# Performance work log

Hardware: AMD Instinct MI355X
Metric: run time of the kernel (lower is better)

The kernel has to match this reference:

```python
import jax, jax.numpy as jnp
import numpy as np

VOCAB = 50257
D_MODEL = 256
HIDDEN = 512
NUM_CLASSES = 2
BATCH = 64
SEQ = 512
PAD_IDX = 0


def setup_inputs() -> dict:
    key = jax.random.key(0)
    ks = jax.random.split(key, 8)
    input_ids = jax.random.randint(ks[0], (BATCH, SEQ), 0, VOCAB)
    emb = jax.random.normal(ks[1], (VOCAB, D_MODEL), dtype=jnp.float32) * 0.02
    emb = emb.at[PAD_IDX].set(0.0)  # padding_idx row is zero
    s_x = 1.0 / np.sqrt(D_MODEL)
    s_h = 1.0 / np.sqrt(HIDDEN)
    Wx = jax.random.uniform(ks[2], (D_MODEL, 3 * HIDDEN), minval=-s_x, maxval=s_x)
    Wh = jax.random.uniform(ks[3], (HIDDEN, 3 * HIDDEN), minval=-s_h, maxval=s_h)
    bx = jax.random.uniform(ks[4], (3 * HIDDEN,), minval=-s_h, maxval=s_h)
    bh = jax.random.uniform(ks[5], (3 * HIDDEN,), minval=-s_h, maxval=s_h)
    Wo = jax.random.uniform(ks[6], (HIDDEN, NUM_CLASSES), minval=-s_h, maxval=s_h)
    bo = jax.random.uniform(ks[7], (NUM_CLASSES,), minval=-s_h, maxval=s_h)
    return {"input_ids": input_ids, "emb": emb, "Wx": Wx, "Wh": Wh,
            "bx": bx, "bh": bh, "Wo": Wo, "bo": bo}


def reference(input_ids, emb, Wx, Wh, bx, bh, Wo, bo):
    # Embedding lookup: [B, S, D]
    x = emb[input_ids]
    # Precompute input-side gate projections for all timesteps: [B, S, 3H]
    xg = jnp.einsum('bsd,dg->bsg', x, Wx) + bx
    H = Wh.shape[0]
    h0 = jnp.zeros((input_ids.shape[0], H), dtype=x.dtype)

    def step(h, xg_t):
        hg = h @ Wh + bh                    # [B, 3H]
        xr, xz, xn = jnp.split(xg_t, 3, axis=-1)
        hr, hz, hn = jnp.split(hg, 3, axis=-1)
        r = jax.nn.sigmoid(xr + hr)
        z = jax.nn.sigmoid(xz + hz)
        n = jnp.tanh(xn + r * hn)
        h_new = (1.0 - z) * n + z * h
        return h_new, None

    # scan over time; only the last hidden state feeds the classifier head
    h_last, _ = jax.lax.scan(step, h0, jnp.swapaxes(xg, 0, 1))
    # Dropout is identity in eval mode (p=0.5 at train time)
    logits = h_last @ Wo + bo               # [B, num_classes]
    return logits
```

## Files before the change

### kernel.cpp

```cpp
#include <hip/hip_runtime.h>
#include <hip/hip_bf16.h>

#define BATCH   64
#define SEQ     512
#define DMODEL  256
#define HIDDEN  512
#define G3      1536
#define NBLK    128
#define UPB     4
#define CPB     12
#define CHUNK   128
#define NCHUNK  4
#define HSLOT   (HIDDEN * BATCH)

typedef unsigned long long u64;
typedef unsigned int u32;

__global__ __launch_bounds__(512) void prep_wh(const float* __restrict__ Wh,
                                               float* __restrict__ whp) {
    int t = blockIdx.x * 512 + threadIdx.x;
    int k   = t & 511;
    int cb  = t >> 9;
    int c   = cb % 12;
    int blk = cb / 12;
    int u = c & 3, g = c >> 2;
    whp[t] = Wh[(long)k * G3 + g * HIDDEN + blk * UPB + u];
}

__global__ void init_flags(unsigned* flags) {
    __hip_atomic_store(&flags[threadIdx.x], 0u, __ATOMIC_RELAXED,
                       __HIP_MEMORY_SCOPE_AGENT);
}

__global__ __launch_bounds__(256) void xg_gemm(const int* __restrict__ ids,
                                               const float* __restrict__ emb,
                                               const float* __restrict__ Wx,
                                               const float* __restrict__ bx,
                                               float* __restrict__ xgC,
                                               int chunk) {
    __shared__ float Es[64][68];
    __shared__ float Ws[64][68];
    __shared__ int   sids[64];

    const int tid = threadIdx.x;
    const int nb = blockIdx.x;
    const int lt = blockIdx.y;
    const int s  = chunk * CHUNK + lt;
    const int tn = tid & 15;
    const int tm = tid >> 4;

    if (tid < 64) sids[tid] = ids[tid * SEQ + s];
    __syncthreads();

    float acc[4][4];
#pragma unroll
    for (int i = 0; i < 4; ++i)
#pragma unroll
        for (int j = 0; j < 4; ++j) acc[i][j] = 0.f;

    for (int kb = 0; kb < 256; kb += 64) {
#pragma unroll
        for (int p = 0; p < 4; ++p) {
            int b = p * 16 + tm;
            float4 av = *(const float4*)(emb + (long)sids[b] * DMODEL + kb + tn * 4);
            Es[tn * 4 + 0][b] = av.x;
            Es[tn * 4 + 1][b] = av.y;
            Es[tn * 4 + 2][b] = av.z;
            Es[tn * 4 + 3][b] = av.w;
            int krow = p * 16 + tm;
            float4 wv = *(const float4*)(Wx + (long)(kb + krow) * G3 + nb * 64 + tn * 4);
            *(float4*)&Ws[krow][tn * 4] = wv;
        }
        __syncthreads();
#pragma unroll
        for (int k = 0; k < 64; ++k) {
            float4 w4 = *(const float4*)&Ws[k][tm * 4];
            float4 e4 = *(const float4*)&Es[k][tn * 4];
            float ww[4] = {w4.x, w4.y, w4.z, w4.w};
            float ee[4] = {e4.x, e4.y, e4.z, e4.w};
#pragma unroll
            for (int i = 0; i < 4; ++i)
#pragma unroll
                for (int j = 0; j < 4; ++j)
                    acc[i][j] = fmaf(ww[i], ee[j], acc[i][j]);
        }
        __syncthreads();
    }

#pragma unroll
    for (int i = 0; i < 4; ++i) {
        int col = nb * 64 + tm * 4 + i;
        float bxi = bx[col];
        float4 o;
        o.x = acc[i][0] + bxi;
        o.y = acc[i][1] + bxi;
        o.z = acc[i][2] + bxi;
        o.w = acc[i][3] + bxi;
        *(float4*)(xgC + (long)col * (CHUNK * BATCH) + lt * 64 + tn * 4) = o;
    }
}

__global__ __launch_bounds__(512, 2) void gru_scan(const float* __restrict__ whp,
                                                   const float* __restrict__ xgC,
                                                   const float* __restrict__ bh,
                                                   float* hist,
                                                   unsigned* flags,
                                                   int chunk) {
    const int tid = threadIdx.x;
    const int blk = blockIdx.x;
    const int b   = tid & 63;
    const int wu  = __builtin_amdgcn_readfirstlane(tid >> 6);

    __shared__ float part[2][8][CPB][64];

    const float* wb = whp + blk * (CPB * HIDDEN) + wu * 64;
    const int base = chunk * CHUNK;

    int jg = 0;
    float bhr = 0.f, bhz = 0.f, bhn = 0.f, hprev = 0.f;
    const float* xr_p = nullptr; const float* xz_p = nullptr; const float* xn_p = nullptr;
    if (wu < 4) {
        jg  = blk * UPB + wu;
        bhr = bh[jg];
        bhz = bh[HIDDEN + jg];
        bhn = bh[2 * HIDDEN + jg];
        xr_p = xgC + (long)jg * (CHUNK * BATCH) + b;
        xz_p = xgC + (long)(HIDDEN + jg) * (CHUNK * BATCH) + b;
        xn_p = xgC + (long)(2 * HIDDEN + jg) * (CHUNK * BATCH) + b;
        hprev = (chunk == 0) ? 0.f : hist[(long)jg * 64 + b];
    }

#pragma unroll 1
    for (int lt = 0; lt < CHUNK; ++lt) {
        const int t  = base + lt;
        const int pb = lt & 1;
        const u32* hq = (const u32*)(hist + (long)lt * HSLOT) + wu * (64 * 64) + b;
        float*     hw = hist + (long)((lt + 1) & (CHUNK - 1)) * HSLOT;

        float xr = 0.f, xz = 0.f, xn = 0.f;
        if (wu < 4) {
            xr = xr_p[lt * 64];
            xz = xz_p[lt * 64];
            xn = xn_p[lt * 64];
        }

        float acc[CPB];
#pragma unroll
        for (int c = 0; c < CPB; ++c) acc[c] = 0.f;

        if (t > 0) {
            if (lt > 0) {
                const u32 tgt = (u32)t;
                for (;;) {
                    u32 f = __hip_atomic_load(&flags[wu * 64 + b], __ATOMIC_RELAXED,
                                              __HIP_MEMORY_SCOPE_AGENT);
                    if (__all((int)(f >= tgt))) break;
                    __builtin_amdgcn_s_sleep(1);
                }
            }
            float hv[64];
#pragma unroll
            for (int i = 0; i < 64; ++i) {
                u32 w = __hip_atomic_load(hq + i * 64, __ATOMIC_RELAXED,
                                          __HIP_MEMORY_SCOPE_AGENT);
                hv[i] = __uint_as_float(w);
            }
            __builtin_amdgcn_sched_barrier(0);
#pragma unroll
            for (int i = 0; i < 64; ++i) {
                const float hvv = hv[i];
#pragma unroll
                for (int c = 0; c < CPB; ++c)
                    acc[c] = fmaf(hvv, wb[c * HIDDEN + i], acc[c]);
            }
        }

#pragma unroll
        for (int c = 0; c < CPB; ++c) part[pb][wu][c][b] = acc[c];
        __syncthreads();

        if (wu < 4) {
            __builtin_amdgcn_s_setprio(1);
            float hgr = bhr, hgz = bhz, hgn = bhn;
#pragma unroll
            for (int ww = 0; ww < 8; ++ww) {
                hgr += part[pb][ww][wu][b];
                hgz += part[pb][ww][4 + wu][b];
                hgn += part[pb][ww][8 + wu][b];
            }
            float r  = 1.f / (1.f + expf(-(xr + hgr)));
            float z  = 1.f / (1.f + expf(-(xz + hgz)));
            float nn = tanhf(xn + r * hgn);
            float hnew = (1.f - z) * nn + z * hprev;
            hprev = hnew;
            __hip_atomic_store((u32*)hw + (long)jg * 64 + b, __float_as_uint(hnew),
                               __ATOMIC_RELAXED, __HIP_MEMORY_SCOPE_AGENT);
            asm volatile("s_waitcnt vmcnt(0)" ::: "memory");
            if (b == 0)
                __hip_atomic_store(&flags[jg], (u32)(t + 1), __ATOMIC_RELAXED,
                                   __HIP_MEMORY_SCOPE_AGENT);
            __builtin_amdgcn_s_setprio(0);
        }
    }
}

__global__ void head_kernel(const float* __restrict__ hist,
                            const float* __restrict__ Wo,
                            const float* __restrict__ bo,
                            float* __restrict__ out) {
    int tid = threadIdx.x;
    int b = tid >> 1, n = tid & 1;
    float acc = bo[n];
#pragma unroll 8
    for (int k = 0; k < HIDDEN; ++k)
        acc = fmaf(hist[(long)k * 64 + b], Wo[k * 2 + n], acc);
    out[b * 2 + n] = acc;
}

extern "C" void kernel_launch(void* const* d_in, const int* in_sizes, int n_in,
                              void* d_out, int out_size, void* d_ws, size_t ws_size,
                              hipStream_t stream) {
    (void)in_sizes; (void)n_in; (void)out_size; (void)ws_size;
    const int*   ids = (const int*)  d_in[0];
    const float* emb = (const float*)d_in[1];
    const float* Wx  = (const float*)d_in[2];
    const float* Wh  = (const float*)d_in[3];
    const float* bx  = (const float*)d_in[4];
    const float* bh  = (const float*)d_in[5];
    const float* Wo  = (const float*)d_in[6];
    const float* bo  = (const float*)d_in[7];
    float* out = (float*)d_out;

    char* ws = (char*)d_ws;
    unsigned* flags = (unsigned*)ws;
    float* hist = (float*)(ws + 2048);
    float* whp  = (float*)(ws + 2048 + (size_t)CHUNK * HSLOT * 4);
    float* xgC  = (float*)(ws + 2048 + (size_t)CHUNK * HSLOT * 4
                           + (size_t)NBLK * CPB * HIDDEN * 4);

    init_flags<<<dim3(1), dim3(512), 0, stream>>>(flags);
    prep_wh<<<dim3(1536), dim3(512), 0, stream>>>(Wh, whp);
    for (int c = 0; c < NCHUNK; ++c) {
        xg_gemm<<<dim3(24, CHUNK), dim3(256), 0, stream>>>(ids, emb, Wx, bx, xgC, c);
        gru_scan<<<dim3(NBLK), dim3(512), 0, stream>>>(whp, xgC, bh, hist, flags, c);
    }
    head_kernel<<<dim3(1), dim3(128), 0, stream>>>(hist, Wo, bo, out);
}
```

Baseline: 5.348 ms.

## Replace store-drain wait with sentinel-poisoned hidden-state slots and retry loads

Result: slower. 5.769 ms (+7.9%).

```diff
diff --git a/kernel.cpp b/kernel.cpp
--- a/kernel.cpp
+++ b/kernel.cpp
@@ -13,11 +13,18 @@
 #define NCHUNK  4
 #define HSLOT   (HIDDEN * BATCH)
 
+#define SENT32  0xFFC00000u
+#define SENT64  0xFFC00000FFC00000ULL
+
 typedef unsigned long long u64;
 typedef unsigned int u32;
 
 __global__ __launch_bounds__(512) void prep_wh(const float* __restrict__ Wh,
-                                               float* __restrict__ whp) {
+                                               float* __restrict__ whp,
+                                               unsigned* flags) {
+    if (blockIdx.x == 0)
+        __hip_atomic_store(&flags[threadIdx.x], 0u, __ATOMIC_RELAXED,
+                           __HIP_MEMORY_SCOPE_AGENT);
     int t = blockIdx.x * 512 + threadIdx.x;
     int k   = t & 511;
     int cb  = t >> 9;
@@ -27,16 +34,12 @@
     whp[t] = Wh[(long)k * G3 + g * HIDDEN + blk * UPB + u];
 }
 
-__global__ void init_flags(unsigned* flags) {
-    __hip_atomic_store(&flags[threadIdx.x], 0u, __ATOMIC_RELAXED,
-                       __HIP_MEMORY_SCOPE_AGENT);
-}
-
 __global__ __launch_bounds__(256) void xg_gemm(const int* __restrict__ ids,
                                                const float* __restrict__ emb,
                                                const float* __restrict__ Wx,
                                                const float* __restrict__ bx,
                                                float* __restrict__ xgC,
+                                               float* __restrict__ hist,
                                                int chunk) {
     __shared__ float Es[64][68];
     __shared__ float Ws[64][68];
@@ -48,6 +51,16 @@
     const int s  = chunk * CHUNK + lt;
     const int tn = tid & 15;
     const int tm = tid >> 4;
+
+    {
+        long gid = ((long)(blockIdx.y * 24 + blockIdx.x)) * 256 + tid;
+        u64* hq = (u64*)(hist + HSLOT);
+#pragma unroll
+        for (int r = 0; r < 3; ++r) {
+            long i = gid + (long)r * 786432;
+            if (i < 2080768) hq[i] = SENT64;
+        }
+    }
 
     if (tid < 64) sids[tid] = ids[tid * SEQ + s];
     __syncthreads();
@@ -158,12 +171,29 @@
                     __builtin_amdgcn_s_sleep(1);
                 }
             }
+            asm volatile("" ::: "memory");
+
             float hv[64];
 #pragma unroll
             for (int i = 0; i < 64; ++i) {
                 u32 w = __hip_atomic_load(hq + i * 64, __ATOMIC_RELAXED,
                                           __HIP_MEMORY_SCOPE_AGENT);
                 hv[i] = __uint_as_float(w);
+            }
+            for (;;) {
+                int anybad = 0;
+#pragma unroll
+                for (int i = 0; i < 64; ++i)
+                    anybad |= (__float_as_uint(hv[i]) == SENT32);
+                if (!__any(anybad)) break;
+#pragma unroll
+                for (int i = 0; i < 64; ++i) {
+                    if (__any((int)(__float_as_uint(hv[i]) == SENT32))) {
+                        u32 w = __hip_atomic_load(hq + i * 64, __ATOMIC_RELAXED,
+                                                  __HIP_MEMORY_SCOPE_AGENT);
+                        hv[i] = __uint_as_float(w);
+                    }
+                }
             }
             __builtin_amdgcn_sched_barrier(0);
 #pragma unroll
@@ -195,7 +225,6 @@
             hprev = hnew;
             __hip_atomic_store((u32*)hw + (long)jg * 64 + b, __float_as_uint(hnew),
                                __ATOMIC_RELAXED, __HIP_MEMORY_SCOPE_AGENT);
-            asm volatile("s_waitcnt vmcnt(0)" ::: "memory");
             if (b == 0)
                 __hip_atomic_store(&flags[jg], (u32)(t + 1), __ATOMIC_RELAXED,
                                    __HIP_MEMORY_SCOPE_AGENT);
@@ -238,10 +267,9 @@
     float* xgC  = (float*)(ws + 2048 + (size_t)CHUNK * HSLOT * 4
                            + (size_t)NBLK * CPB * HIDDEN * 4);
 
-    init_flags<<<dim3(1), dim3(512), 0, stream>>>(flags);
-    prep_wh<<<dim3(1536), dim3(512), 0, stream>>>(Wh, whp);
+    prep_wh<<<dim3(1536), dim3(512), 0, stream>>>(Wh, whp, flags);
     for (int c = 0; c < NCHUNK; ++c) {
-        xg_gemm<<<dim3(24, CHUNK), dim3(256), 0, stream>>>(ids, emb, Wx, bx, xgC, c);
+        xg_gemm<<<dim3(24, CHUNK), dim3(256), 0, stream>>>(ids, emb, Wx, bx, xgC, hist, c);
         gru_scan<<<dim3(NBLK), dim3(512), 0, stream>>>(whp, xgC, bh, hist, flags, c);
     }
     head_kernel<<<dim3(1), dim3(128), 0, stream>>>(hist, Wo, bo, out);
```
